# Kernel optimization log

Hardware: AMD Instinct MI355X
Metric: run time of the kernel (lower is better)

## Reference

```python
import jax, jax.numpy as jnp
import numpy as np

Y = 1      # init kwarg y
DIM = 2    # init kwarg dim


def setup_inputs() -> dict:
    key = jax.random.key(0)
    k1, k2, k3 = jax.random.split(key, 3)
    B, L = 16, 512
    H = 32
    x = jax.random.normal(k1, (B, L, L), dtype=jnp.float32)
    # xavier_uniform-like init for weights
    lim1 = np.sqrt(6.0 / (3 + H)).astype(np.float32)
    W1 = jax.random.uniform(k2, (H, 3), dtype=jnp.float32, minval=-lim1, maxval=lim1)
    b1 = jnp.zeros((H,), dtype=jnp.float32)
    lim2 = np.sqrt(6.0 / (H + 1)).astype(np.float32)
    W2 = jax.random.uniform(k3, (1, H), dtype=jnp.float32, minval=-lim2, maxval=lim2)
    b2 = jnp.zeros((1,), dtype=jnp.float32)
    return {"x": x, "W1": W1, "b1": b1, "W2": W2, "b2": b2}


def reference(x, W1, b1, W2, b2):
    # nearest-neighbor sum along both lattice dims
    x1 = (jnp.roll(x, 1, axis=1) + jnp.roll(x, -1, axis=1)
          + jnp.roll(x, 1, axis=2) + jnp.roll(x, -1, axis=2))
    # shifted-by-y neighbor sum along DIM
    sx = jnp.roll(x, Y, axis=DIM) + jnp.roll(x, -Y, axis=DIM)
    # per-site 3-feature vector: [x^2, x1*x, sx*x] -> (B, L, L, 3)
    inp = jnp.stack([x * x, x1 * x, sx * x], axis=-1)
    # tiny pointwise MLP 3 -> 32 -> 1
    h = jnp.tanh(jnp.einsum('blmf,hf->blmh', inp, W1) + b1)
    out = jnp.einsum('blmh,oh->blmo', h, W2)[..., 0] + b2[0]
    # sum over lattice sites -> per-config scalar (B,)
    return out.sum(axis=(1, 2))
```

## Files before the change

### kernel.cpp

```cpp
#include <hip/hip_runtime.h>

#define L 512
#define LMASK 511
#define HID 32

constexpr int THREADS        = 256;
constexpr int ROWS_PER_BLOCK = 4;
constexpr int BLOCKS_PER_B   = L / ROWS_PER_BLOCK;
constexpr int NTAB           = 5376;

constexpr float MAGIC   = 8388608.0f;
constexpr float CLAMPLO = 8388608.0f;
constexpr float CLAMPHI = 8410108.0f;

__global__ __launch_bounds__(THREADS)
void site_kernel(const float* __restrict__ x,
                 const float* __restrict__ W1,
                 const float* __restrict__ b1,
                 const float* __restrict__ W2,
                 float* __restrict__ partial) {
    __shared__ __align__(16) float tab_s[NTAB];
    __shared__ __align__(16) float zw_s[128];
    __shared__ __align__(16) float w2_s[HID];

    const int t = threadIdx.x;

    if (t < HID) {
        const float K256 = 256.0f * 2.8853900817779268f;
        const int g = t >> 2, q = t & 3;
        zw_s[g * 16 +  0 + q] = K256 * W1[t * 3 + 0];
        zw_s[g * 16 +  4 + q] = K256 * W1[t * 3 + 1];
        zw_s[g * 16 +  8 + q] = K256 * W1[t * 3 + 2];
        zw_s[g * 16 + 12 + q] = fmaf(K256, b1[t], 5378.0f + MAGIC);
        w2_s[t] = -2.0f * W2[t];
    }
    for (int i = t; i < NTAB; i += THREADS) {
        const float zp = fmaf((float)i, 0.015625f, -21.0f);
        tab_s[i] = __builtin_amdgcn_rcpf(1.0f + __builtin_amdgcn_exp2f(zp));
    }
    __syncthreads();

    const int blk = blockIdx.x;
    const int b   = blk >> 7;
    const int i0  = (blk & (BLOCKS_PER_B - 1)) * ROWS_PER_BLOCK;
    const float* __restrict__ xb = x + (size_t)b * (L * L);

    float F0[8], F1[8], F2[8];
#pragma unroll
    for (int g = 0; g < 2; ++g) {
        const int j  = t + g * THREADS;
        const int jm = (j + LMASK) & LMASK, jp = (j + 1) & LMASK;

        float cc[6];
#pragma unroll
        for (int r = 0; r < 6; ++r) {
            const int i = (i0 + r - 1 + L) & LMASK;
            cc[r] = xb[i * L + j];
        }
#pragma unroll
        for (int s = 0; s < 4; ++s) {
            const int i   = i0 + s;
            const float lf = xb[i * L + jm];
            const float rg = xb[i * L + jp];
            const float c  = cc[s + 1];
            const float lr = lf + rg;
            const float x1 = lr + cc[s] + cc[s + 2];
            const int k = g * 4 + s;
            F0[k] = c * c;  F1[k] = x1 * c;  F2[k] = lr * c;
        }
    }

    float acc[8] = {0.f, 0.f, 0.f, 0.f, 0.f, 0.f, 0.f, 0.f};
    const char* __restrict__ tb = (const char*)tab_s;

#pragma unroll 1
    for (int gq = 0; gq < 8; ++gq) {
        const float4 wa  = *(const float4*)&zw_s[gq * 16 + 0];
        const float4 wb  = *(const float4*)&zw_s[gq * 16 + 4];
        const float4 wc  = *(const float4*)&zw_s[gq * 16 + 8];
        const float4 w0  = *(const float4*)&zw_s[gq * 16 + 12];
        const float4 w2v = *(const float4*)&w2_s[gq * 4];
#pragma unroll
        for (int q = 0; q < 4; ++q) {
            const float waq = ((const float*)&wa)[q];
            const float wbq = ((const float*)&wb)[q];
            const float wcq = ((const float*)&wc)[q];
            const float w0q = ((const float*)&w0)[q];
            const float w2q = ((const float*)&w2v)[q];
#pragma unroll
            for (int s = 0; s < 8; ++s) {
                const float uu = fmaf(F0[s], waq, fmaf(F1[s], wbq, fmaf(F2[s], wcq, w0q)));
                const float uc = __builtin_amdgcn_fmed3f(uu, CLAMPLO, CLAMPHI);
                const int  off = __float_as_int(uc) & 0x007FFFFC;
                const float y  = *reinterpret_cast<const float*>(tb + off);
                acc[s] = fmaf(w2q, y, acc[s]);
            }
        }
    }

    float a = ((acc[0] + acc[1]) + (acc[2] + acc[3]))
            + ((acc[4] + acc[5]) + (acc[6] + acc[7]));
#pragma unroll
    for (int off = 32; off > 0; off >>= 1)
        a += __shfl_down(a, off, 64);

    __shared__ float wsum[THREADS / 64];
    const int wid = t >> 6, lane = t & 63;
    if (lane == 0) wsum[wid] = a;
    __syncthreads();
    if (t == 0)
        partial[blk] = (wsum[0] + wsum[1]) + (wsum[2] + wsum[3]);
}

__global__ __launch_bounds__(128)
void reduce_kernel(const float* __restrict__ partial,
                   const float* __restrict__ W2,
                   const float* __restrict__ b2,
                   float* __restrict__ out) {
    const int b = blockIdx.x, t = threadIdx.x;
    const float NS = (float)(L * L);

    float v = partial[b * BLOCKS_PER_B + t];
    if (t < HID) v += NS * W2[t];
    if (t == 0)  v += NS * b2[0];

#pragma unroll
    for (int off = 32; off > 0; off >>= 1)
        v += __shfl_down(v, off, 64);

    __shared__ float ws2[2];
    if ((t & 63) == 0) ws2[t >> 6] = v;
    __syncthreads();
    if (t == 0) out[b] = ws2[0] + ws2[1];
}

extern "C" void kernel_launch(void* const* d_in, const int* in_sizes, int n_in,
                              void* d_out, int out_size, void* d_ws, size_t ws_size,
                              hipStream_t stream) {
    const float* x  = (const float*)d_in[0];
    const float* W1 = (const float*)d_in[1];
    const float* b1 = (const float*)d_in[2];
    const float* W2 = (const float*)d_in[3];
    const float* b2 = (const float*)d_in[4];
    float* out      = (float*)d_out;
    float* partial  = (float*)d_ws;

    const int B = in_sizes[0] / (L * L);

    site_kernel<<<B * BLOCKS_PER_B, THREADS, 0, stream>>>(x, W1, b1, W2, partial);
    reduce_kernel<<<B, 128, 0, stream>>>(partial, W2, b2, out);
}
```

Baseline: 35.58 us.

## Split hidden units between LDS sigmoid table and exact exp/rcp pairs

Only 20 of the 32 hidden units now go through the shared-memory lookup table. The other 12 are evaluated directly with exp2 and rcp, processed in pairs so each pair shares a single reciprocal. The table shrinks from 5376 to 2048 entries with a narrower clamp range. The goal is to move part of the LDS-gather work onto the VALU/transcendental units, balancing LDS bandwidth against ALU throughput. In exchange, clamping tanh inputs to a narrower table range may add approximation error for large pre-activations.

```diff
diff --git a/kernel.cpp b/kernel.cpp
--- a/kernel.cpp
+++ b/kernel.cpp
@@ -7,11 +7,13 @@
 constexpr int THREADS        = 256;
 constexpr int ROWS_PER_BLOCK = 4;
 constexpr int BLOCKS_PER_B   = L / ROWS_PER_BLOCK;
-constexpr int NTAB           = 5376;
+constexpr int NTAB           = 2048;
+constexpr int GT             = 5;
+constexpr int NPAIR_E        = 6;
 
 constexpr float MAGIC   = 8388608.0f;
 constexpr float CLAMPLO = 8388608.0f;
-constexpr float CLAMPHI = 8410108.0f;
+constexpr float CLAMPHI = 8396796.0f;
 
 __global__ __launch_bounds__(THREADS)
 void site_kernel(const float* __restrict__ x,
@@ -20,22 +22,34 @@
                  const float* __restrict__ W2,
                  float* __restrict__ partial) {
     __shared__ __align__(16) float tab_s[NTAB];
-    __shared__ __align__(16) float zw_s[128];
-    __shared__ __align__(16) float w2_s[HID];
+    __shared__ __align__(16) float zw_s[GT * 16];
+    __shared__ __align__(16) float w2t_s[GT * 4];
+    __shared__ __align__(16) float ew_s[NPAIR_E * 8];
+    __shared__ __align__(8)  float ew2_s[NPAIR_E * 2];
 
     const int t = threadIdx.x;
+    const float Ke = 2.8853900817779268f;
 
     if (t < HID) {
-        const float K256 = 256.0f * 2.8853900817779268f;
-        const int g = t >> 2, q = t & 3;
-        zw_s[g * 16 +  0 + q] = K256 * W1[t * 3 + 0];
-        zw_s[g * 16 +  4 + q] = K256 * W1[t * 3 + 1];
-        zw_s[g * 16 +  8 + q] = K256 * W1[t * 3 + 2];
-        zw_s[g * 16 + 12 + q] = fmaf(K256, b1[t], 5378.0f + MAGIC);
-        w2_s[t] = -2.0f * W2[t];
+        if (t < 4 * GT) {
+            const float K256 = 256.0f * Ke;
+            const int g = t >> 2, q = t & 3;
+            zw_s[g * 16 +  0 + q] = K256 * W1[t * 3 + 0];
+            zw_s[g * 16 +  4 + q] = K256 * W1[t * 3 + 1];
+            zw_s[g * 16 +  8 + q] = K256 * W1[t * 3 + 2];
+            zw_s[g * 16 + 12 + q] = fmaf(K256, b1[t], 4098.0f + MAGIC);
+            w2t_s[t] = -2.0f * W2[t];
+        } else {
+            const int e = t - 4 * GT, p = e >> 1, q = e & 1;
+            ew_s[p * 8 + 0 + q] = Ke * W1[t * 3 + 0];
+            ew_s[p * 8 + 2 + q] = Ke * W1[t * 3 + 1];
+            ew_s[p * 8 + 4 + q] = Ke * W1[t * 3 + 2];
+            ew_s[p * 8 + 6 + q] = Ke * b1[t];
+            ew2_s[p * 2 + q]    = -2.0f * W2[t];
+        }
     }
     for (int i = t; i < NTAB; i += THREADS) {
-        const float zp = fmaf((float)i, 0.015625f, -21.0f);
+        const float zp = fmaf((float)i, 0.015625f, -16.001953125f);
         tab_s[i] = __builtin_amdgcn_rcpf(1.0f + __builtin_amdgcn_exp2f(zp));
     }
     __syncthreads();
@@ -74,12 +88,12 @@
     const char* __restrict__ tb = (const char*)tab_s;
 
 #pragma unroll 1
-    for (int gq = 0; gq < 8; ++gq) {
+    for (int gq = 0; gq < GT; ++gq) {
         const float4 wa  = *(const float4*)&zw_s[gq * 16 + 0];
         const float4 wb  = *(const float4*)&zw_s[gq * 16 + 4];
         const float4 wc  = *(const float4*)&zw_s[gq * 16 + 8];
         const float4 w0  = *(const float4*)&zw_s[gq * 16 + 12];
-        const float4 w2v = *(const float4*)&w2_s[gq * 4];
+        const float4 w2v = *(const float4*)&w2t_s[gq * 4];
 #pragma unroll
         for (int q = 0; q < 4; ++q) {
             const float waq = ((const float*)&wa)[q];
@@ -95,6 +109,27 @@
                 const float y  = *reinterpret_cast<const float*>(tb + off);
                 acc[s] = fmaf(w2q, y, acc[s]);
             }
+        }
+    }
+
+#pragma unroll 1
+    for (int p = 0; p < NPAIR_E; ++p) {
+        const float4 e0 = *(const float4*)&ew_s[p * 8 + 0];
+        const float4 e1 = *(const float4*)&ew_s[p * 8 + 4];
+        const float2 w2p = *(const float2*)&ew2_s[p * 2];
+        const float wa0 = e0.x, wa1 = e0.y, wb0 = e0.z, wb1 = e0.w;
+        const float wc0 = e1.x, wc1 = e1.y, w00 = e1.z, w01 = e1.w;
+#pragma unroll
+        for (int s = 0; s < 8; ++s) {
+            float z0 = fmaf(F0[s], wa0, fmaf(F1[s], wb0, fmaf(F2[s], wc0, w00)));
+            float z1 = fmaf(F0[s], wa1, fmaf(F1[s], wb1, fmaf(F2[s], wc1, w01)));
+            z0 = __builtin_amdgcn_fmed3f(z0, -30.0f, 30.0f);
+            z1 = __builtin_amdgcn_fmed3f(z1, -30.0f, 30.0f);
+            const float d0 = 1.0f + __builtin_amdgcn_exp2f(z0);
+            const float d1 = 1.0f + __builtin_amdgcn_exp2f(z1);
+            const float nm = fmaf(w2p.x, d1, w2p.y * d0);
+            const float rr = __builtin_amdgcn_rcpf(d0 * d1);
+            acc[s] = fmaf(nm, rr, acc[s]);
         }
     }
 
```

Result: faster. 34.09 us (-4.2%).

## Replace LDS sigmoid lookup table with paired exp2/rcp using packed FP32 math

Applied to the files above, without the earlier changes.

Drops the per-block 5376-entry shared-memory sigmoid table and its per-element LDS gathers. Each hidden unit's tanh term is now computed directly with exp2, and two hidden units are combined over a common denominator so one reciprocal serves both. The arithmetic is written with two-wide float vectors so the compiler can emit packed FP32 FMA/mul/add. In exchange, transcendental work rises to two exp2 plus one rcp per unit pair per site, and table-build and LDS traffic go away.

```diff
diff --git a/kernel.cpp b/kernel.cpp
--- a/kernel.cpp
+++ b/kernel.cpp
@@ -7,11 +7,9 @@
 constexpr int THREADS        = 256;
 constexpr int ROWS_PER_BLOCK = 4;
 constexpr int BLOCKS_PER_B   = L / ROWS_PER_BLOCK;
-constexpr int NTAB           = 5376;
+constexpr int NPAIR          = HID / 2;
 
-constexpr float MAGIC   = 8388608.0f;
-constexpr float CLAMPLO = 8388608.0f;
-constexpr float CLAMPHI = 8410108.0f;
+using v2f = __attribute__((ext_vector_type(2))) float;
 
 __global__ __launch_bounds__(THREADS)
 void site_kernel(const float* __restrict__ x,
@@ -19,24 +17,19 @@
                  const float* __restrict__ b1,
                  const float* __restrict__ W2,
                  float* __restrict__ partial) {
-    __shared__ __align__(16) float tab_s[NTAB];
-    __shared__ __align__(16) float zw_s[128];
-    __shared__ __align__(16) float w2_s[HID];
+    __shared__ __align__(16) float ew_s[NPAIR * 8];
+    __shared__ __align__(8)  float ew2_s[NPAIR * 2];
 
     const int t = threadIdx.x;
+    const float Ke = 2.8853900817779268f;
 
     if (t < HID) {
-        const float K256 = 256.0f * 2.8853900817779268f;
-        const int g = t >> 2, q = t & 3;
-        zw_s[g * 16 +  0 + q] = K256 * W1[t * 3 + 0];
-        zw_s[g * 16 +  4 + q] = K256 * W1[t * 3 + 1];
-        zw_s[g * 16 +  8 + q] = K256 * W1[t * 3 + 2];
-        zw_s[g * 16 + 12 + q] = fmaf(K256, b1[t], 5378.0f + MAGIC);
-        w2_s[t] = -2.0f * W2[t];
-    }
-    for (int i = t; i < NTAB; i += THREADS) {
-        const float zp = fmaf((float)i, 0.015625f, -21.0f);
-        tab_s[i] = __builtin_amdgcn_rcpf(1.0f + __builtin_amdgcn_exp2f(zp));
+        const int p = t >> 1, q = t & 1;
+        ew_s[p * 8 + 0 + q] = Ke * W1[t * 3 + 0];
+        ew_s[p * 8 + 2 + q] = Ke * W1[t * 3 + 1];
+        ew_s[p * 8 + 4 + q] = Ke * W1[t * 3 + 2];
+        ew_s[p * 8 + 6 + q] = Ke * b1[t];
+        ew2_s[p * 2 + q]    = -2.0f * W2[t];
     }
     __syncthreads();
 
@@ -70,36 +63,53 @@
         }
     }
 
-    float acc[8] = {0.f, 0.f, 0.f, 0.f, 0.f, 0.f, 0.f, 0.f};
-    const char* __restrict__ tb = (const char*)tab_s;
+    v2f F0v[4], F1v[4], F2v[4];
+#pragma unroll
+    for (int d = 0; d < 4; ++d) {
+        F0v[d] = v2f{F0[2 * d], F0[2 * d + 1]};
+        F1v[d] = v2f{F1[2 * d], F1[2 * d + 1]};
+        F2v[d] = v2f{F2[2 * d], F2[2 * d + 1]};
+    }
+
+    v2f acc0 = {0.f, 0.f}, acc1 = {0.f, 0.f}, acc2 = {0.f, 0.f}, acc3 = {0.f, 0.f};
+    const v2f one = {1.0f, 1.0f};
 
 #pragma unroll 1
-    for (int gq = 0; gq < 8; ++gq) {
-        const float4 wa  = *(const float4*)&zw_s[gq * 16 + 0];
-        const float4 wb  = *(const float4*)&zw_s[gq * 16 + 4];
-        const float4 wc  = *(const float4*)&zw_s[gq * 16 + 8];
-        const float4 w0  = *(const float4*)&zw_s[gq * 16 + 12];
-        const float4 w2v = *(const float4*)&w2_s[gq * 4];
+    for (int p = 0; p < NPAIR; ++p) {
+        const float4 e0 = *(const float4*)&ew_s[p * 8 + 0];
+        const float4 e1 = *(const float4*)&ew_s[p * 8 + 4];
+        const float2 wp = *(const float2*)&ew2_s[p * 2];
+        const v2f waa0 = {e0.x, e0.x}, waa1 = {e0.y, e0.y};
+        const v2f wbb0 = {e0.z, e0.z}, wbb1 = {e0.w, e0.w};
+        const v2f wcc0 = {e1.x, e1.x}, wcc1 = {e1.y, e1.y};
+        const v2f w000 = {e1.z, e1.z}, w001 = {e1.w, e1.w};
+        const v2f w2xx = {wp.x, wp.x}, w2yy = {wp.y, wp.y};
+
 #pragma unroll
-        for (int q = 0; q < 4; ++q) {
-            const float waq = ((const float*)&wa)[q];
-            const float wbq = ((const float*)&wb)[q];
-            const float wcq = ((const float*)&wc)[q];
-            const float w0q = ((const float*)&w0)[q];
-            const float w2q = ((const float*)&w2v)[q];
-#pragma unroll
-            for (int s = 0; s < 8; ++s) {
-                const float uu = fmaf(F0[s], waq, fmaf(F1[s], wbq, fmaf(F2[s], wcq, w0q)));
-                const float uc = __builtin_amdgcn_fmed3f(uu, CLAMPLO, CLAMPHI);
-                const int  off = __float_as_int(uc) & 0x007FFFFC;
-                const float y  = *reinterpret_cast<const float*>(tb + off);
-                acc[s] = fmaf(w2q, y, acc[s]);
-            }
+        for (int d = 0; d < 4; ++d) {
+            const v2f z0 = __builtin_elementwise_fma(F0v[d], waa0,
+                           __builtin_elementwise_fma(F1v[d], wbb0,
+                           __builtin_elementwise_fma(F2v[d], wcc0, w000)));
+            const v2f z1 = __builtin_elementwise_fma(F0v[d], waa1,
+                           __builtin_elementwise_fma(F1v[d], wbb1,
+                           __builtin_elementwise_fma(F2v[d], wcc1, w001)));
+            const v2f ex0 = {__builtin_amdgcn_exp2f(z0.x), __builtin_amdgcn_exp2f(z0.y)};
+            const v2f ex1 = {__builtin_amdgcn_exp2f(z1.x), __builtin_amdgcn_exp2f(z1.y)};
+            const v2f d0 = ex0 + one;
+            const v2f d1 = ex1 + one;
+            const v2f nm = __builtin_elementwise_fma(w2yy, d0, w2xx * d1);
+            const v2f D  = d0 * d1;
+            const v2f rr = {__builtin_amdgcn_rcpf(D.x), __builtin_amdgcn_rcpf(D.y)};
+            const v2f contrib = nm * rr;
+            if      (d == 0) acc0 += contrib;
+            else if (d == 1) acc1 += contrib;
+            else if (d == 2) acc2 += contrib;
+            else             acc3 += contrib;
         }
     }
 
-    float a = ((acc[0] + acc[1]) + (acc[2] + acc[3]))
-            + ((acc[4] + acc[5]) + (acc[6] + acc[7]));
+    float a = ((acc0.x + acc0.y) + (acc1.x + acc1.y))
+            + ((acc2.x + acc2.y) + (acc3.x + acc3.y));
 #pragma unroll
     for (int off = 32; off > 0; off >>= 1)
         a += __shfl_down(a, off, 64);
```

Measured after the change: 32.47 us. 8.7% less time.
